# Kernel tuning notes

Hardware: AMD Instinct MI355X
Metric: run time of the kernel (lower is better)

Reference implementation:

```python
import jax, jax.numpy as jnp
import numpy as np

B, C_IN, C_OUT, M, K1, K2 = 8, 256, 256, 4096, 4, 4


def _cheb_assemble(K, L, x):
    # x: (B, C_in, M) -> X: (B, C_in, M, K) with X[..., k] = L^k x
    # Batched as a single (M, M) @ (M, B*C_in) GEMM per power step.
    Bv, Cv, Mv = x.shape
    x0 = x.reshape(Bv * Cv, Mv).T  # (M, B*C_in)

    def step(carry, _):
        return L @ carry, carry  # emit L^k x, carry becomes L^{k+1} x

    _, ys = jax.lax.scan(step, x0, None, length=K)  # (K, M, B*C_in)
    return ys.transpose(2, 1, 0).reshape(Bv, Cv, Mv, K)


def setup_inputs() -> dict:
    key = jax.random.key(0)
    k1, k2, k3, k4 = jax.random.split(key, 4)
    scale = 1.0 / np.sqrt(M)  # keep spectral radius O(1) so L^k stays finite
    Ll = jax.random.normal(k1, (M, M), dtype=jnp.float32) * scale
    Lu = jax.random.normal(k2, (M, M), dtype=jnp.float32) * scale
    x = jax.random.normal(k3, (B, C_IN, M), dtype=jnp.float32)
    theta1 = jax.random.normal(k4, (C_OUT, C_IN, K1 + K2), dtype=jnp.float32)  # variance=1.0
    bias1 = jnp.zeros((1, C_OUT, 1), dtype=jnp.float32)
    return {"Ll": Ll, "Lu": Lu, "x": x, "theta1": theta1, "bias1": bias1}


def reference(Ll, Lu, x, theta1, bias1):
    X1 = _cheb_assemble(K1, Ll, x)  # (B, C_in, M, K1)
    X2 = _cheb_assemble(K2, Lu, x)  # (B, C_in, M, K2)
    X = jnp.concatenate((X1, X2), axis=3)  # (B, C_in, M, K1+K2)
    y = jnp.einsum("bimk,oik->bom", X, theta1)
    return y + bias1  # (B, C_out, M)
```

## Files before the change

kernel.cpp:

```cpp
#include <hip/hip_runtime.h>
#include <hip/hip_bf16.h>

typedef __hip_bfloat16 bf16;
typedef __attribute__((ext_vector_type(8))) short bshort8;
typedef __attribute__((ext_vector_type(4))) float f32x4;

#define GLL16(gsrc, ldst)                                                      \
  __builtin_amdgcn_global_load_lds(                                            \
      (const __attribute__((address_space(1))) void*)(gsrc),                   \
      (__attribute__((address_space(3))) void*)(ldst), 16, 0, 0)

#define MEMFENCE asm volatile("" ::: "memory")
#define BARRIER                                                                \
  do {                                                                         \
    MEMFENCE;                                                                  \
    __builtin_amdgcn_s_barrier();                                              \
    MEMFENCE;                                                                  \
  } while (0)
#define WAIT_LGKM0 asm volatile("s_waitcnt lgkmcnt(0)" ::: "memory")
#define WAIT_LGKM8 asm volatile("s_waitcnt lgkmcnt(8)" ::: "memory")
#define WAIT_VM(n) asm volatile("s_waitcnt vmcnt(" #n ")" ::: "memory")

__global__ __launch_bounds__(256) void cast_f32_bf16(const float* __restrict__ src,
                                                     bf16* __restrict__ dst, int n4) {
  int stride = gridDim.x * blockDim.x;
  const float4* s4 = reinterpret_cast<const float4*>(src);
  __hip_bfloat162* d2 = reinterpret_cast<__hip_bfloat162*>(dst);
  for (int i = blockIdx.x * blockDim.x + threadIdx.x; i < n4; i += stride) {
    float4 v = s4[i];
    d2[2 * i]     = __float22bfloat162_rn(make_float2(v.x, v.y));
    d2[2 * i + 1] = __float22bfloat162_rn(make_float2(v.z, v.w));
  }
}

__global__ __launch_bounds__(256) void transpose_cast_x(const float* __restrict__ x,
                                                        bf16* __restrict__ Xt) {
  __shared__ bf16 t[64][65];
  int b = blockIdx.z;
  int m0 = blockIdx.x * 64;
  int i0 = blockIdx.y * 64;
  int tx = threadIdx.x & 63;
  int ty = threadIdx.x >> 6;
  for (int ii = ty; ii < 64; ii += 4)
    t[ii][tx] = __float2bfloat16(x[(size_t)(b * 256 + i0 + ii) * 4096 + m0 + tx]);
  __syncthreads();
  for (int mm = ty; mm < 64; mm += 4)
    Xt[(size_t)(b * 4096 + m0 + mm) * 256 + i0 + tx] = t[tx][mm];
}

__global__ __launch_bounds__(256) void build_theta(const float* __restrict__ th,
                                                   bf16* __restrict__ Tall) {
  int idx = blockIdx.x * 256 + threadIdx.x;
  int s = idx >> 16;
  int oi = idx & 65535;
  float v;
  if (s == 0)      v = th[oi * 8 + 0] + th[oi * 8 + 4];
  else if (s <= 3) v = th[oi * 8 + s];
  else             v = th[oi * 8 + s + 1];
  Tall[idx] = __float2bfloat16(v);
}

__device__ __forceinline__ void gemm_bt_tile(const bf16* __restrict__ A,
                                             const bf16* __restrict__ Bm, int K,
                                             bf16* __restrict__ Cb) {
  __shared__ __align__(16) bf16 As[128 * 32];
  __shared__ __align__(16) bf16 Bs[128 * 32];
  const int tid = threadIdx.x;
  const int lane = tid & 63;
  const int w = tid >> 6;
  const int wr = w >> 1, wc = w & 1;

  const int srow = w * 32 + (lane >> 2);
  const int scol = (lane & 3) * 8;
  bf16* ldsA0 = &As[(w * 32 + 0) * 32];
  bf16* ldsA1 = &As[(w * 32 + 16) * 32];
  bf16* ldsB0 = &Bs[(w * 32 + 0) * 32];
  bf16* ldsB1 = &Bs[(w * 32 + 16) * 32];
  const bf16* aptr0 = A + (size_t)srow * K + scol;
  const bf16* aptr1 = A + (size_t)(srow + 16) * K + scol;
  const bf16* bptr0 = Bm + (size_t)srow * K + scol;
  const bf16* bptr1 = Bm + (size_t)(srow + 16) * K + scol;

  f32x4 acc[4][4];
#pragma unroll
  for (int i = 0; i < 4; ++i)
#pragma unroll
    for (int j = 0; j < 4; ++j) acc[i][j] = (f32x4){0.f, 0.f, 0.f, 0.f};

  const int rsel = lane & 15;
  const int ksel = (lane >> 4) * 8;

  for (int kt = 0; kt < K; kt += 32) {
    GLL16(aptr0 + kt, ldsA0);
    GLL16(aptr1 + kt, ldsA1);
    GLL16(bptr0 + kt, ldsB0);
    GLL16(bptr1 + kt, ldsB1);
    __syncthreads();
    bshort8 av[4], bv[4];
#pragma unroll
    for (int m = 0; m < 4; ++m)
      av[m] = *reinterpret_cast<const bshort8*>(&As[(wr * 64 + m * 16 + rsel) * 32 + ksel]);
#pragma unroll
    for (int n = 0; n < 4; ++n)
      bv[n] = *reinterpret_cast<const bshort8*>(&Bs[(wc * 64 + n * 16 + rsel) * 32 + ksel]);
#pragma unroll
    for (int m = 0; m < 4; ++m)
#pragma unroll
      for (int n = 0; n < 4; ++n)
        acc[m][n] = __builtin_amdgcn_mfma_f32_16x16x32_bf16(av[m], bv[n], acc[m][n], 0, 0, 0);
    __syncthreads();
  }

  const int colf = lane & 15;
  const int rowf = (lane >> 4) * 4;
#pragma unroll
  for (int m = 0; m < 4; ++m) {
#pragma unroll
    for (int n = 0; n < 4; ++n) {
      int r0 = wr * 64 + m * 16 + rowf;
      int c = wc * 64 + n * 16 + colf;
#pragma unroll
      for (int r = 0; r < 4; ++r) {
        size_t off = (size_t)(r0 + r) * 4096 + c;
        Cb[off] = __float2bfloat16(acc[m][n][r]);
      }
    }
  }
}

__global__ __launch_bounds__(256) void chan_all(const bf16* __restrict__ Tall,
                                                const bf16* __restrict__ Xt,
                                                bf16* __restrict__ U0,
                                                bf16* __restrict__ U1,
                                                bf16* __restrict__ U2,
                                                bf16* __restrict__ U3) {
  int rt = blockIdx.x;
  int ct = blockIdx.y;
  int z = blockIdx.z;
  int slot, b;
  bf16* Ubuf;
  size_t rowbase;
  if (z < 48) {
    int k = 1 + z / 16;
    int r = z % 16;
    int chain = r >> 3;
    b = r & 7;
    slot = chain ? k + 3 : k;
    Ubuf = (k == 1) ? U1 : ((k == 2) ? U2 : U3);
    rowbase = (size_t)(chain * 2048 + b * 256);
  } else {
    b = z - 48;
    slot = 0;
    Ubuf = U0;
    rowbase = (size_t)b * 256;
  }
  const bf16* A = Tall + (size_t)slot * 65536 + (size_t)rt * 128 * 256;
  const bf16* Bm = Xt + (size_t)b * 4096 * 256 + (size_t)ct * 128 * 256;
  bf16* dst = Ubuf + (rowbase + (size_t)rt * 128) * 4096 + ct * 128;
  gemm_bt_tile(A, Bm, 256, dst);
}

template <int EPI>
__global__ __launch_bounds__(512, 2) void gemm256(
    const bf16* __restrict__ Aall, const bf16* __restrict__ B0m,
    const bf16* __restrict__ B1m, bf16* __restrict__ Cb, float* __restrict__ Cf,
    float* __restrict__ Cf2, const bf16* __restrict__ Db,
    const float* __restrict__ bias, int K) {
  const int tid = threadIdx.x;
  const int lane = tid & 63;
  const int w = tid >> 6;
  const int wr = w >> 2, wc = w & 3;

  int bid = blockIdx.x;
  int gid = (bid & 7) * 32 + (bid >> 3);
  const int rt = gid >> 4, ct = gid & 15;

  const bf16* Atile = Aall + (size_t)rt * 256 * K;
  const bf16* Btile = ((rt < 8) ? B0m : B1m) + (size_t)ct * 256 * K;

  __shared__ __align__(16) char lds_[131072];

  const int srow = tid >> 3;
  const int scol = (((tid & 7) ^ (srow & 7)) << 3);
  const bf16* gA = Atile + (size_t)srow * K + scol;
  const bf16* gB = Btile + (size_t)srow * K + scol;

#define STAGE_A(buf, half, kt)                                                 \
  do {                                                                         \
    char* l = &lds_[(buf)*65536 + (half)*16384 + w * 1024];                    \
    const bf16* g = gA + (size_t)((half)*128) * K + (size_t)(kt)*64;           \
    GLL16(g, l);                                                               \
    GLL16(g + (size_t)64 * K, l + 8192);                                       \
  } while (0)
#define STAGE_B(buf, half, kt)                                                 \
  do {                                                                         \
    char* l = &lds_[(buf)*65536 + 32768 + (half)*16384 + w * 1024];            \
    const bf16* g = gB + (size_t)((half)*128) * K + (size_t)(kt)*64;           \
    GLL16(g, l);                                                               \
    GLL16(g + (size_t)64 * K, l + 8192);                                       \
  } while (0)

  const int rsel = lane & 15;
  const int cbb = lane >> 4;
  const int xorv = rsel & 7;
  const int aBase = wr * 16384 + rsel * 128;
  const int bBase = 32768 + (wc >> 1) * 16384 + ((wc & 1) * 64 + rsel) * 128;
#define LDA(buf, mf, ks)                                                       \
  (*(const bshort8*)&lds_[(buf)*65536 + aBase + (mf)*2048 +                    \
                          (((((ks)*4) + cbb) ^ xorv) << 4)])
#define LDB(buf, nf, ks)                                                       \
  (*(const bshort8*)&lds_[(buf)*65536 + bBase + (nf)*2048 +                    \
                          (((((ks)*4) + cbb) ^ xorv) << 4)])

  f32x4 acc[8][4];
#pragma unroll
  for (int i = 0; i < 8; ++i)
#pragma unroll
    for (int j = 0; j < 4; ++j) acc[i][j] = (f32x4){0.f, 0.f, 0.f, 0.f};

  const int NT = K >> 6;
  const int NI = NT >> 1;

  bshort8 afr[2][2];
  bshort8 bfr[4][2];

#define RD_A(BUF, Q)                                                           \
  do {                                                                         \
    afr[0][0] = LDA(BUF, (Q)*2 + 0, 0); afr[0][1] = LDA(BUF, (Q)*2 + 0, 1);    \
    afr[1][0] = LDA(BUF, (Q)*2 + 1, 0); afr[1][1] = LDA(BUF, (Q)*2 + 1, 1);    \
  } while (0)
#define RD_B4(BUF)                                                             \
  do {                                                                         \
    bfr[0][0] = LDB(BUF, 0, 0); bfr[0][1] = LDB(BUF, 0, 1);                    \
    bfr[1][0] = LDB(BUF, 1, 0); bfr[1][1] = LDB(BUF, 1, 1);                    \
    bfr[2][0] = LDB(BUF, 2, 0); bfr[2][1] = LDB(BUF, 2, 1);                    \
    bfr[3][0] = LDB(BUF, 3, 0); bfr[3][1] = LDB(BUF, 3, 1);                    \
  } while (0)

#define MFMA16(Q)                                                              \
  do {                                                                         \
    _Pragma("unroll") for (int mi = 0; mi < 2; ++mi)                           \
    _Pragma("unroll") for (int nf = 0; nf < 4; ++nf)                           \
    _Pragma("unroll") for (int ks = 0; ks < 2; ++ks)                           \
        acc[(Q)*2 + mi][nf] = __builtin_amdgcn_mfma_f32_16x16x32_bf16(         \
            afr[mi][ks], bfr[nf][ks], acc[(Q)*2 + mi][nf], 0, 0, 0);           \
  } while (0)

#define PHA(BUF, Q, RDB, STAGESTMT, TAILSTMT)                                  \
  do {                                                                         \
    if (RDB) RD_B4(BUF);                                                       \
    RD_A(BUF, Q);                                                              \
    STAGESTMT;                                                                 \
    if (RDB) WAIT_LGKM8;                                                       \
    BARRIER;                                                                   \
    WAIT_LGKM0;                                                                \
    __builtin_amdgcn_s_setprio(1);                                             \
    MFMA16(Q);                                                                 \
    __builtin_amdgcn_s_setprio(0);                                             \
    TAILSTMT;                                                                  \
    BARRIER;                                                                   \
  } while (0)

  STAGE_B(0, 0, 0); STAGE_B(0, 1, 0);
  STAGE_A(0, 0, 0); STAGE_A(0, 1, 0);
  STAGE_B(1, 0, 1); STAGE_B(1, 1, 1);
  WAIT_VM(4);
  BARRIER;

  for (int it = 0; it < NI - 1; ++it) {
    const int t1 = 2 * it + 1, t2 = 2 * it + 2, t3 = 2 * it + 3;
    PHA(0, 0, 1, { STAGE_A(1, 0, t1); STAGE_A(1, 1, t1); }, {});
    PHA(0, 1, 0, { STAGE_B(0, 0, t2); }, {});
    PHA(0, 2, 0, { STAGE_B(0, 1, t2); }, {});
    PHA(0, 3, 0, {}, { WAIT_VM(4); });
    PHA(1, 0, 1, { STAGE_A(0, 0, t2); }, {});
    PHA(1, 1, 0, { STAGE_A(0, 1, t2); }, {});
    PHA(1, 2, 0, { STAGE_B(1, 0, t3); }, {});
    PHA(1, 3, 0, { STAGE_B(1, 1, t3); }, { WAIT_VM(4); });
  }
  {
    const int tl = NT - 1;
    PHA(0, 0, 1, { STAGE_A(1, 0, tl); STAGE_A(1, 1, tl); }, {});
    PHA(0, 1, 0, {}, {});
    PHA(0, 2, 0, {}, {});
    PHA(0, 3, 0, {}, { WAIT_VM(0); });
    PHA(1, 0, 1, {}, {});
    PHA(1, 1, 0, {}, {});
    PHA(1, 2, 0, {}, {});
    PHA(1, 3, 0, {}, {});
  }

  const int colf = lane & 15;
  const int rowf = (lane >> 4) * 4;
  const size_t crow0 = (size_t)rt * 256 + wr * 128;
  const size_t ccol0 = (size_t)ct * 256 + wc * 64;
#pragma unroll
  for (int mf = 0; mf < 8; ++mf) {
#pragma unroll
    for (int nf = 0; nf < 4; ++nf) {
#pragma unroll
      for (int r = 0; r < 4; ++r) {
        size_t row = crow0 + mf * 16 + rowf + r;
        size_t col = ccol0 + nf * 16 + colf;
        size_t off = row * 4096 + col;
        float v = acc[mf][nf][r];
        if constexpr (EPI == 0) {
          v += __bfloat162float(Db[off]);
          Cb[off] = __float2bfloat16(v);
        } else {
          if (rt < 8) {
            v += __bfloat162float(Db[off]) + bias[row & 255];
            Cf[off] = v;
          } else {
            Cf2[(row - 2048) * 4096 + col] = v;
          }
        }
      }
    }
  }
#undef STAGE_A
#undef STAGE_B
#undef LDA
#undef LDB
#undef RD_A
#undef RD_B4
#undef MFMA16
#undef PHA
}

__global__ __launch_bounds__(256) void reduce_add(float* __restrict__ Y,
                                                  const float* __restrict__ P1) {
  float4* Y4 = (float4*)Y;
  const float4* P4 = (const float4*)P1;
  const int n4 = 2048 * 4096 / 4;
  int stride = gridDim.x * blockDim.x;
  for (int i = blockIdx.x * 256 + threadIdx.x; i < n4; i += stride) {
    float4 a = Y4[i];
    float4 b = P4[i];
    a.x += b.x; a.y += b.y; a.z += b.z; a.w += b.w;
    Y4[i] = a;
  }
}

extern "C" void kernel_launch(void* const* d_in, const int* in_sizes, int n_in,
                              void* d_out, int out_size, void* d_ws, size_t ws_size,
                              hipStream_t stream) {
  const float* Ll = (const float*)d_in[0];
  const float* Lu = (const float*)d_in[1];
  const float* x = (const float*)d_in[2];
  const float* th = (const float*)d_in[3];
  const float* bias = (const float*)d_in[4];
  float* Y = (float*)d_out;

  char* ws = (char*)d_ws;
  const size_t SZ_L = (size_t)4096 * 4096 * 2;
  const size_t SZ_U = (size_t)4096 * 4096 * 2;
  const size_t SZ_X = (size_t)8 * 4096 * 256 * 2;
  const size_t SZ_T = ((size_t)7 * 256 * 256 * 2 + 255) & ~(size_t)255;
  const size_t SZ_U0 = (size_t)2048 * 4096 * 2;
  bf16* Llb = (bf16*)ws; ws += SZ_L;
  bf16* Lub = (bf16*)ws; ws += SZ_L;
  bf16* Xt  = (bf16*)ws; ws += SZ_X;
  bf16* Tall = (bf16*)ws; ws += SZ_T;
  bf16* U1 = (bf16*)ws; ws += SZ_U;
  bf16* U2 = (bf16*)ws; ws += SZ_U;
  bf16* U3 = (bf16*)ws; ws += SZ_U;
  bf16* U0 = (bf16*)ws; ws += SZ_U0;
  bf16* V1 = (bf16*)ws; ws += SZ_U;
  float* P1 = (float*)V1;
  (void)ws_size; (void)in_sizes; (void)n_in; (void)out_size;

  cast_f32_bf16<<<2048, 256, 0, stream>>>(Ll, Llb, 4096 * 4096 / 4);
  cast_f32_bf16<<<2048, 256, 0, stream>>>(Lu, Lub, 4096 * 4096 / 4);
  transpose_cast_x<<<dim3(64, 4, 8), 256, 0, stream>>>(x, Xt);
  build_theta<<<1792, 256, 0, stream>>>(th, Tall);

  chan_all<<<dim3(2, 32, 56), 256, 0, stream>>>(Tall, Xt, U0, U1, U2, U3);

  gemm256<0><<<256, 512, 0, stream>>>(U3, Llb, Lub, V1, nullptr, nullptr, U2,
                                      nullptr, 4096);
  gemm256<0><<<256, 512, 0, stream>>>(V1, Llb, Lub, U3, nullptr, nullptr, U1,
                                      nullptr, 4096);
  gemm256<2><<<256, 512, 0, stream>>>(U3, Llb, Lub, nullptr, Y, P1, U0, bias,
                                      4096);
  reduce_add<<<2048, 256, 0, stream>>>(Y, P1);
}
```

Baseline: 494.8 us.

## Double-buffer B fragments in registers and prefetch next tile's B across phases

Splits the B register fragments into two sets. While the MFMAs for the current k-tile run on one set, the next tile's B pairs are read from LDS into the other set, one pair per phase. This replaces the bulk B read and lgkmcnt(8) wait at the start of each half. Global staging is regrouped so both halves of an operand are issued in one phase, and the vmcnt waits are tightened to zero. The aim is to hide LDS read latency behind MFMA work, at the cost of about 32 extra VGPRs and less global-load overlap from the stricter vmcnt(0) waits.

```diff
diff --git a/kernel.cpp b/kernel.cpp
--- a/kernel.cpp
+++ b/kernel.cpp
@@ -18,7 +18,7 @@
     MEMFENCE;                                                                  \
   } while (0)
 #define WAIT_LGKM0 asm volatile("s_waitcnt lgkmcnt(0)" ::: "memory")
-#define WAIT_LGKM8 asm volatile("s_waitcnt lgkmcnt(8)" ::: "memory")
+#define WAIT_LGKM2 asm volatile("s_waitcnt lgkmcnt(2)" ::: "memory")
 #define WAIT_VM(n) asm volatile("s_waitcnt vmcnt(" #n ")" ::: "memory")
 
 __global__ __launch_bounds__(256) void cast_f32_bf16(const float* __restrict__ src,
@@ -222,40 +222,56 @@
   const int NI = NT >> 1;
 
   bshort8 afr[2][2];
-  bshort8 bfr[4][2];
+  bshort8 bs0[4][2], bs1[4][2];
 
 #define RD_A(BUF, Q)                                                           \
   do {                                                                         \
     afr[0][0] = LDA(BUF, (Q)*2 + 0, 0); afr[0][1] = LDA(BUF, (Q)*2 + 0, 1);    \
     afr[1][0] = LDA(BUF, (Q)*2 + 1, 0); afr[1][1] = LDA(BUF, (Q)*2 + 1, 1);    \
   } while (0)
-#define RD_B4(BUF)                                                             \
-  do {                                                                         \
-    bfr[0][0] = LDB(BUF, 0, 0); bfr[0][1] = LDB(BUF, 0, 1);                    \
-    bfr[1][0] = LDB(BUF, 1, 0); bfr[1][1] = LDB(BUF, 1, 1);                    \
-    bfr[2][0] = LDB(BUF, 2, 0); bfr[2][1] = LDB(BUF, 2, 1);                    \
-    bfr[3][0] = LDB(BUF, 3, 0); bfr[3][1] = LDB(BUF, 3, 1);                    \
-  } while (0)
-
-#define MFMA16(Q)                                                              \
+#define RD_PAIR(SET, BUF, Q)                                                   \
+  do {                                                                         \
+    SET[Q][0] = LDB(BUF, Q, 0);                                                \
+    SET[Q][1] = LDB(BUF, Q, 1);                                                \
+  } while (0)
+#define RD_B8(SET, BUF)                                                        \
+  do {                                                                         \
+    SET[0][0] = LDB(BUF, 0, 0); SET[0][1] = LDB(BUF, 0, 1);                    \
+    SET[1][0] = LDB(BUF, 1, 0); SET[1][1] = LDB(BUF, 1, 1);                    \
+    SET[2][0] = LDB(BUF, 2, 0); SET[2][1] = LDB(BUF, 2, 1);                    \
+    SET[3][0] = LDB(BUF, 3, 0); SET[3][1] = LDB(BUF, 3, 1);                    \
+  } while (0)
+
+#define MFMA16(Q, BSET)                                                        \
   do {                                                                         \
     _Pragma("unroll") for (int mi = 0; mi < 2; ++mi)                           \
     _Pragma("unroll") for (int nf = 0; nf < 4; ++nf)                           \
     _Pragma("unroll") for (int ks = 0; ks < 2; ++ks)                           \
         acc[(Q)*2 + mi][nf] = __builtin_amdgcn_mfma_f32_16x16x32_bf16(         \
-            afr[mi][ks], bfr[nf][ks], acc[(Q)*2 + mi][nf], 0, 0, 0);           \
-  } while (0)
-
-#define PHA(BUF, Q, RDB, STAGESTMT, TAILSTMT)                                  \
-  do {                                                                         \
-    if (RDB) RD_B4(BUF);                                                       \
-    RD_A(BUF, Q);                                                              \
+            afr[mi][ks], BSET[nf][ks], acc[(Q)*2 + mi][nf], 0, 0, 0);          \
+  } while (0)
+
+#define PH(ABUF, Q, BSET, RDNXT, STAGESTMT, TAILSTMT)                          \
+  do {                                                                         \
+    RD_A(ABUF, Q);                                                             \
+    RDNXT;                                                                     \
     STAGESTMT;                                                                 \
-    if (RDB) WAIT_LGKM8;                                                       \
+    BARRIER;                                                                   \
+    WAIT_LGKM2;                                                                \
+    __builtin_amdgcn_s_setprio(1);                                             \
+    MFMA16(Q, BSET);                                                           \
+    __builtin_amdgcn_s_setprio(0);                                             \
+    TAILSTMT;                                                                  \
+    BARRIER;                                                                   \
+  } while (0)
+#define PHL(ABUF, Q, BSET, STAGESTMT, TAILSTMT)                                \
+  do {                                                                         \
+    RD_A(ABUF, Q);                                                             \
+    STAGESTMT;                                                                 \
     BARRIER;                                                                   \
     WAIT_LGKM0;                                                                \
     __builtin_amdgcn_s_setprio(1);                                             \
-    MFMA16(Q);                                                                 \
+    MFMA16(Q, BSET);                                                           \
     __builtin_amdgcn_s_setprio(0);                                             \
     TAILSTMT;                                                                  \
     BARRIER;                                                                   \
@@ -264,30 +280,31 @@
   STAGE_B(0, 0, 0); STAGE_B(0, 1, 0);
   STAGE_A(0, 0, 0); STAGE_A(0, 1, 0);
   STAGE_B(1, 0, 1); STAGE_B(1, 1, 1);
-  WAIT_VM(4);
+  WAIT_VM(0);
   BARRIER;
+  RD_B8(bs0, 0);
 
   for (int it = 0; it < NI - 1; ++it) {
     const int t1 = 2 * it + 1, t2 = 2 * it + 2, t3 = 2 * it + 3;
-    PHA(0, 0, 1, { STAGE_A(1, 0, t1); STAGE_A(1, 1, t1); }, {});
-    PHA(0, 1, 0, { STAGE_B(0, 0, t2); }, {});
-    PHA(0, 2, 0, { STAGE_B(0, 1, t2); }, {});
-    PHA(0, 3, 0, {}, { WAIT_VM(4); });
-    PHA(1, 0, 1, { STAGE_A(0, 0, t2); }, {});
-    PHA(1, 1, 0, { STAGE_A(0, 1, t2); }, {});
-    PHA(1, 2, 0, { STAGE_B(1, 0, t3); }, {});
-    PHA(1, 3, 0, { STAGE_B(1, 1, t3); }, { WAIT_VM(4); });
+    PH(0, 0, bs0, RD_PAIR(bs1, 1, 0), { STAGE_A(1, 0, t1); STAGE_A(1, 1, t1); }, {});
+    PH(0, 1, bs0, RD_PAIR(bs1, 1, 1), { STAGE_B(0, 0, t2); STAGE_B(0, 1, t2); }, {});
+    PH(0, 2, bs0, RD_PAIR(bs1, 1, 2), {}, {});
+    PH(0, 3, bs0, RD_PAIR(bs1, 1, 3), {}, { WAIT_VM(0); });
+    PH(1, 0, bs1, RD_PAIR(bs0, 0, 0), { STAGE_A(0, 0, t2); STAGE_A(0, 1, t2); }, {});
+    PH(1, 1, bs1, RD_PAIR(bs0, 0, 1), { STAGE_B(1, 0, t3); STAGE_B(1, 1, t3); }, {});
+    PH(1, 2, bs1, RD_PAIR(bs0, 0, 2), {}, {});
+    PH(1, 3, bs1, RD_PAIR(bs0, 0, 3), {}, { WAIT_VM(0); });
   }
   {
     const int tl = NT - 1;
-    PHA(0, 0, 1, { STAGE_A(1, 0, tl); STAGE_A(1, 1, tl); }, {});
-    PHA(0, 1, 0, {}, {});
-    PHA(0, 2, 0, {}, {});
-    PHA(0, 3, 0, {}, { WAIT_VM(0); });
-    PHA(1, 0, 1, {}, {});
-    PHA(1, 1, 0, {}, {});
-    PHA(1, 2, 0, {}, {});
-    PHA(1, 3, 0, {}, {});
+    PH(0, 0, bs0, RD_PAIR(bs1, 1, 0), { STAGE_A(1, 0, tl); STAGE_A(1, 1, tl); }, {});
+    PH(0, 1, bs0, RD_PAIR(bs1, 1, 1), {}, {});
+    PH(0, 2, bs0, RD_PAIR(bs1, 1, 2), {}, {});
+    PH(0, 3, bs0, RD_PAIR(bs1, 1, 3), {}, { WAIT_VM(0); });
+    PHL(1, 0, bs1, {}, {});
+    PHL(1, 1, bs1, {}, {});
+    PHL(1, 2, bs1, {}, {});
+    PHL(1, 3, bs1, {}, {});
   }
 
   const int colf = lane & 15;
@@ -323,9 +340,11 @@
 #undef LDA
 #undef LDB
 #undef RD_A
-#undef RD_B4
+#undef RD_PAIR
+#undef RD_B8
 #undef MFMA16
-#undef PHA
+#undef PH
+#undef PHL
 }
 
 __global__ __launch_bounds__(256) void reduce_add(float* __restrict__ Y,
```

New measurement: 670.6 us. 1.36x slower.
